# Performance work log

Hardware: AMD Instinct MI355X
Metric: run time of the kernel (lower is better)

Reference implementation:

```python
import jax, jax.numpy as jnp
import numpy as np

LAM = 0.5  # self.lam_
N, T, C, H, W = 8, 8, 128, 64, 64


def setup_inputs() -> dict:
    key = jax.random.key(0)
    k1, k2, k3, k4 = jax.random.split(key, 4)
    x = jax.random.normal(k1, (N, T, C, H, W), dtype=jnp.float32)
    # Conv2d(2,1,k=3,p=1,bias=False) weights: [out=1, in=2, 3, 3]
    w_conv1 = jax.random.normal(k2, (1, 2, 3, 3), dtype=jnp.float32) * 0.1
    w_conv2 = jax.random.normal(k3, (1, 2, 3, 3), dtype=jnp.float32) * 0.1
    # Conv3d(2T, T, k=3, p=1, bias=False): [out=T, in=2T, 3, 3, 3]
    w_conv_last = jax.random.normal(k4, (T, 2 * T, 3, 3, 3), dtype=jnp.float32) * 0.05
    return {"x": x, "w_conv1": w_conv1, "w_conv2": w_conv2, "w_conv_last": w_conv_last}


def _conv2d_same(y, wgt):
    # y: [B, 2, H, W], wgt: [1, 2, 3, 3] -> [B, 1, H, W]
    return jax.lax.conv_general_dilated(
        y, wgt, window_strides=(1, 1), padding=[(1, 1), (1, 1)],
        dimension_numbers=("NCHW", "OIHW", "NCHW"))


def reference(x, w_conv1, w_conv2, w_conv_last):
    n, t, c, h, w = x.shape
    kc = int(c * LAM)
    kt = int(t * LAM)

    # pooled importance map: avg + max over spatial -> [n, t, c]
    M = jnp.mean(x, axis=(3, 4)) + jnp.max(x, axis=(3, 4))

    # --- channel top-k mask ---
    # Faithful to the torch fancy-index scatter loop: important_channels[:, i, topk_[:, i]] = 1
    # broadcasts the write over ALL batch rows, i.e. a per-timestep union over the batch.
    _, topk_c = jax.lax.top_k(M, kc)                                  # [n, t, kc]
    t_ids = jnp.broadcast_to(jnp.arange(t)[None, :, None], topk_c.shape)
    mask_ch = jnp.zeros((t, c), x.dtype).at[t_ids.ravel(), topk_c.ravel()].set(1.0)  # [t, c]

    # --- time top-k mask (on transposed map) ---
    _, topk_t = jax.lax.top_k(jnp.swapaxes(M, 1, 2), kt)              # [n, c, kt]
    c_ids = jnp.broadcast_to(jnp.arange(c)[None, :, None], topk_t.shape)
    mask_tm = jnp.zeros((c, t), x.dtype).at[c_ids.ravel(), topk_t.ravel()].set(1.0).T  # [t, c]

    # important iff (mask_ch + mask_tm)/2 == 0.5  <=> XOR of the two masks
    imp = jnp.where(mask_ch + mask_tm == 1.0, 1.0, 0.0).astype(x.dtype)  # [t, c]
    imp = imp[None, :, :, None, None]                                    # [1, t, c, 1, 1]

    im_feat = imp * x
    sub_feat = x - im_feat  # (1 - imp) * x

    im_avg = jnp.mean(im_feat, axis=2, keepdims=True) / LAM           # [n, t, 1, h, w]
    im_max = jnp.max(im_feat, axis=2, keepdims=True)
    sub_avg = jnp.mean(sub_feat, axis=2, keepdims=True) / (1.0 - LAM)
    sub_max = jnp.max(sub_feat, axis=2, keepdims=True)

    im_x = jnp.concatenate([im_avg, im_max], axis=2)                  # [n, t, 2, h, w]
    sub_x = jnp.concatenate([sub_avg, sub_max], axis=2)

    # SeqToANNContainer flattens (t, n) then conv2d per-sample; flatten order irrelevant.
    im_map = jax.nn.sigmoid(_conv2d_same(im_x.reshape(n * t, 2, h, w), w_conv1)).reshape(n, t, 1, h, w)
    sub_map = jax.nn.sigmoid(_conv2d_same(sub_x.reshape(n * t, 2, h, w), w_conv2)).reshape(n, t, 1, h, w)

    htsa = jnp.concatenate([im_map * im_feat, sub_map * sub_feat], axis=1)  # [n, 2t, c, h, w]

    # Conv3d(2t -> t, k=3, p=1): treats t as channels, c as depth
    out = jax.lax.conv_general_dilated(
        htsa, w_conv_last, window_strides=(1, 1, 1),
        padding=[(1, 1), (1, 1), (1, 1)],
        dimension_numbers=("NCDHW", "OIDHW", "NCDHW"))
    return out  # [n, t, c, h, w]
```

## Files before the change

kernel.cpp:

```cpp
#include <hip/hip_runtime.h>
#include <math.h>

#define NN 8
#define TT 8
#define CC 128
#define HH 64
#define WW 64
#define HW 4096

typedef unsigned int u32;
typedef unsigned short u16;
typedef __attribute__((ext_vector_type(8))) short short8;
typedef __attribute__((ext_vector_type(4))) float floatx4;

__device__ __forceinline__ u16 f2bf(float f){
    u32 u = __float_as_uint(f);
    u32 r = (u + 0x7fffu + ((u >> 16) & 1u)) >> 16;
    return (u16)r;
}
__device__ __forceinline__ float bf2f(u16 h){
    return __uint_as_float(((u32)h) << 16);
}

__global__ __launch_bounds__(256) void k1_M(const float* __restrict__ x, float* __restrict__ M){
    int plane = blockIdx.x * 4 + (threadIdx.x >> 6);
    int lane  = threadIdx.x & 63;
    const float* p = x + (size_t)plane * HW;
    float s = 0.f, mx = -INFINITY;
    #pragma unroll
    for (int it = 0; it < 16; ++it){
        float4 v = *(const float4*)(p + it*256 + lane*4);
        s += v.x + v.y + v.z + v.w;
        mx = fmaxf(mx, fmaxf(fmaxf(v.x, v.y), fmaxf(v.z, v.w)));
    }
    #pragma unroll
    for (int off = 32; off > 0; off >>= 1){
        s += __shfl_xor(s, off, 64);
        mx = fmaxf(mx, __shfl_xor(mx, off, 64));
    }
    if (lane == 0) M[plane] = s * (1.0f/(float)HW) + mx;
}

__global__ __launch_bounds__(128) void k2_imp(const float* __restrict__ M, float* __restrict__ imp){
    int t = blockIdx.x;
    int c = threadIdx.x;
    __shared__ float Ms[NN*CC];
    for (int n = 0; n < NN; ++n)
        Ms[n*CC + c] = M[(n*TT + t)*CC + c];
    __syncthreads();
    bool sel_ch = false;
    for (int n = 0; n < NN; ++n){
        float mv = Ms[n*CC + c];
        int rank = 0;
        for (int c2 = 0; c2 < CC; ++c2){
            float v2 = Ms[n*CC + c2];
            rank += (v2 > mv) || (v2 == mv && c2 < c);
        }
        sel_ch = sel_ch || (rank < 64);
    }
    bool sel_tm = false;
    for (int n = 0; n < NN; ++n){
        float mv = M[(n*TT + t)*CC + c];
        int rank = 0;
        for (int t2 = 0; t2 < TT; ++t2){
            float v2 = M[(n*TT + t2)*CC + c];
            rank += (v2 > mv) || (v2 == mv && t2 < t);
        }
        sel_tm = sel_tm || (rank < 4);
    }
    imp[t*CC + c] = (sel_ch != sel_tm) ? 1.0f : 0.0f;
}

__global__ __launch_bounds__(512) void k3a_stats(const float* __restrict__ x,
        const float* __restrict__ imp, u16* __restrict__ st){
    int nt = blockIdx.x; int t = nt & 7;
    int px = blockIdx.y * 512 + threadIdx.x;
    const float* xp = x + (size_t)nt * CC * HW + px;
    float sa = 0.f, sb = 0.f, ma = -INFINITY, mb = -INFINITY;
    for (int c = 0; c < CC; ++c){
        float ip = imp[t*CC + c];
        float v = xp[c*HW];
        float a = ip*v, b = v - a;
        sa += a; sb += b;
        ma = fmaxf(ma, a); mb = fmaxf(mb, b);
    }
    st[(nt*4+0)*HW + px] = f2bf(sa * (1.f/64.f));
    st[(nt*4+1)*HW + px] = f2bf(ma);
    st[(nt*4+2)*HW + px] = f2bf(sb * (1.f/64.f));
    st[(nt*4+3)*HW + px] = f2bf(mb);
}

__global__ __launch_bounds__(256) void k3b_maps(const u16* __restrict__ st,
        const float* __restrict__ w1, const float* __restrict__ w2,
        float* __restrict__ maps){
    int nt = blockIdx.x;
    int y0 = blockIdx.y * 16;
    __shared__ float S[4*18*66];
    int tid = threadIdx.x;
    for (int idx = tid; idx < 4*18*66; idx += 256){
        int s  = idx / 1188;
        int r  = (idx % 1188) / 66;
        int xx = idx % 66;
        int gy = y0 - 1 + r, gx = xx - 1;
        float v = 0.f;
        if ((u32)gy < HH && (u32)gx < WW)
            v = bf2f(st[(nt*4 + s)*HW + gy*WW + gx]);
        S[idx] = v;
    }
    __syncthreads();
    float wa[18], wb[18];
    #pragma unroll
    for (int i = 0; i < 18; ++i){ wa[i] = w1[i]; wb[i] = w2[i]; }
    for (int k = 0; k < 4; ++k){
        int p = k*256 + tid;
        int y = p >> 6, xx = p & 63;
        float zi = 0.f, zs = 0.f;
        #pragma unroll
        for (int dy = 0; dy < 3; ++dy)
            #pragma unroll
            for (int dx = 0; dx < 3; ++dx){
                int sp = (y+dy)*66 + xx + dx;
                zi += wa[dy*3+dx] * S[sp] + wa[9+dy*3+dx] * S[1188 + sp];
                zs += wb[dy*3+dx] * S[2376 + sp] + wb[9+dy*3+dx] * S[3564 + sp];
            }
        maps[(nt*2+0)*HW + y0*WW + p] = 1.0f / (1.0f + expf(-zi));
        maps[(nt*2+1)*HW + y0*WW + p] = 1.0f / (1.0f + expf(-zs));
    }
}

__global__ __launch_bounds__(256) void k4_xs(const float* __restrict__ x,
        const float* __restrict__ impf, const float* __restrict__ maps,
        u16* __restrict__ xs){
    int c = blockIdx.x;
    int n = blockIdx.y;
    int tid = threadIdx.x;
    const float* mp[TT];
    #pragma unroll
    for (int t = 0; t < TT; ++t){
        float v = impf[t*CC + c];
        mp[t] = maps + ((size_t)((n*TT + t)*2) + (v > 0.f ? 0 : 1)) * HW;
    }
    const float* xb = x + ((size_t)(n*TT)*CC + c) * HW;
    u16* xr = xs + ((size_t)n*CC + c) * HW * 8;
    for (int it = 0; it < 16; ++it){
        int p = it*256 + tid;
        union { u16 h[8]; uint4 v4; } r;
        #pragma unroll
        for (int t = 0; t < TT; ++t){
            float xv = xb[(size_t)t*CC*HW + p];
            r.h[t] = f2bf(xv * mp[t][p]);
        }
        *(uint4*)(xr + (size_t)p*8) = r.v4;
    }
}

__global__ __launch_bounds__(64) void kW_frag(const float* __restrict__ wlast,
        const float* __restrict__ impf, u16* __restrict__ fw){
    int c_out = blockIdx.x;
    int stp   = blockIdx.y;
    int lane  = threadIdx.x;
    int m = lane & 15, q = lane >> 4;
    int tap = 4*stp + q;
    int dc = tap / 9;
    int c_in = c_out - 1 + dc;
    bool valid = (m < 8) && (tap < 27) && ((u32)c_in < CC);
    union { u16 h[8]; uint4 v; } pk;
    #pragma unroll
    for (int j = 0; j < 8; ++j){
        float wv = 0.f;
        if (valid){
            int idx = (impf[j*CC + c_in] > 0.f) ? j : j + 8;
            wv = wlast[(m*16 + idx)*27 + tap];
        }
        pk.h[j] = f2bf(wv);
    }
    *(uint4*)(fw + (((size_t)c_out*7 + stp)*64 + lane)*8) = pk.v;
}

constexpr int offb16(int tap){
    return (((tap/9)*6 + ((tap/3)%3))*66 + (tap%3))*16;
}

__global__ __launch_bounds__(256, 6) void k5_fold(
        const u16* __restrict__ xs, const u16* __restrict__ fw,
        float* __restrict__ out){
    __shared__ __align__(16) u16 ft[1584*8];
    int tid  = threadIdx.x;
    int lane = tid & 63;
    int w    = tid >> 6;
    int c0 = blockIdx.x * 2;
    int y0 = blockIdx.y * 4;
    int n  = blockIdx.z;
    int cl = w & 1;
    int c_out = c0 + cl;

    short8 afr[7];
    const u16* fwb = fw + ((size_t)c_out*7*64 + lane)*8;
    #pragma unroll
    for (int stp = 0; stp < 7; ++stp)
        afr[stp] = *(const short8*)(fwb + stp*512);

    for (int idx = tid; idx < 1584; idx += 256){
        int cc  = idx / 396;
        int rm  = idx % 396;
        int yyl = rm / 66;
        int xx  = rm % 66;
        int gc = c0 - 1 + cc;
        int gy = y0 - 1 + yyl;
        int gx = xx - 1;
        uint4 v = make_uint4(0,0,0,0);
        if ((u32)gc < CC && (u32)gy < HH && (u32)gx < WW)
            v = *(const uint4*)(xs + (((size_t)n*CC + gc)*HW + gy*WW + gx)*8);
        *(uint4*)(ft + idx*8) = v;
    }
    __syncthreads();

    int col = lane & 15;
    int q   = lane >> 4;
    const char* fb = (const char*)ft;
    int offs[7];
    #pragma unroll
    for (int stp = 0; stp < 7; ++stp){
        int tap = 4*stp + q;
        if (tap >= 27) tap = 0;
        offs[stp] = offb16(tap);
    }
    for (int yy = 0; yy < 2; ++yy){
        int yl = (w >> 1)*2 + yy;
        int rowb = ((cl*6 + yl)*66 + col)*16;
        #pragma unroll
        for (int xp = 0; xp < 2; ++xp){
            int b0off = rowb + xp*512;
            int b1off = b0off + 256;
            floatx4 acc0 = {0.f,0.f,0.f,0.f};
            floatx4 acc1 = {0.f,0.f,0.f,0.f};
            #pragma unroll
            for (int stp = 0; stp < 7; ++stp){
                short8 b0 = *(const short8*)(fb + b0off + offs[stp]);
                short8 b1 = *(const short8*)(fb + b1off + offs[stp]);
                acc0 = __builtin_amdgcn_mfma_f32_16x16x32_bf16(afr[stp], b0, acc0, 0, 0, 0);
                acc1 = __builtin_amdgcn_mfma_f32_16x16x32_bf16(afr[stp], b1, acc1, 0, 0, 0);
            }
            if (lane < 32){
                int y = y0 + yl;
                int xa = xp*32 + col;
                #pragma unroll
                for (int rg = 0; rg < 4; ++rg){
                    int o = (lane >> 4)*4 + rg;
                    size_t ob = (((size_t)(n*TT + o))*CC + c_out)*HW + y*WW;
                    out[ob + xa]      = acc0[rg];
                    out[ob + xa + 16] = acc1[rg];
                }
            }
        }
    }
}

template<bool USE_XS>
__global__ __launch_bounds__(256) void k5_conv3d(
        const float* __restrict__ x, const u16* __restrict__ xs,
        const float* __restrict__ impf, const float* __restrict__ wlast,
        const float* __restrict__ maps, float* __restrict__ out){
    __shared__ __align__(16) u16 fim[1584*8];
    __shared__ __align__(16) u16 fsb[1584*8];
    __shared__ u32 maskw[CC*4];
    int tid  = threadIdx.x;
    int lane = tid & 63;
    int w    = tid >> 6;
    int c0 = blockIdx.x * 2;
    int y0 = blockIdx.y * 4;
    int n  = blockIdx.z;

    for (int idx = tid; idx < CC*4; idx += 256){
        int c = idx >> 2, j = idx & 3;
        u32 m = (impf[(2*j)*CC + c]   > 0.f ? 0x0000FFFFu : 0u)
              | (impf[(2*j+1)*CC + c] > 0.f ? 0xFFFF0000u : 0u);
        maskw[idx] = m;
    }

    for (int idx = tid; idx < 896; idx += 256){
        int stp = idx >> 6;
        int l   = idx & 63;
        int m = l & 15, q = l >> 4;
        int i0 = (q & 1) * 8, s = q >> 1;
        int tap = 2*stp + s;
        bool valid = (m < 8) && (tap < 27);
        union { u16 h[8]; uint4 v; } pk;
        #pragma unroll
        for (int j = 0; j < 8; ++j){
            float wv = valid ? wlast[(m*16 + i0 + j)*27 + tap] : 0.f;
            pk.h[j] = f2bf(wv);
        }
        *(uint4*)(fim + idx*8) = pk.v;
    }
    __syncthreads();
    short8 afr[14];
    #pragma unroll
    for (int stp = 0; stp < 14; ++stp)
        afr[stp] = *(const short8*)(fim + (stp*64 + lane)*8);
    __syncthreads();

    for (int idx = tid; idx < 1584; idx += 256){
        int cc  = idx / 396;
        int rm  = idx % 396;
        int yyl = rm / 66;
        int xx  = rm % 66;
        int gc = c0 - 1 + cc;
        int gy = y0 - 1 + yyl;
        int gx = xx - 1;
        uint4 vim = make_uint4(0,0,0,0), vsb = make_uint4(0,0,0,0);
        if ((u32)gc < CC && (u32)gy < HH && (u32)gx < WW){
            int gp = gy*WW + gx;
            u32 al[4];
            if (USE_XS){
                uint4 v = *(const uint4*)(xs + (((size_t)n*CC + gc)*HW + gp)*8);
                al[0] = v.x; al[1] = v.y; al[2] = v.z; al[3] = v.w;
            } else {
                const float* xn  = x    + (((size_t)(n*TT))*CC + gc)*HW + gp;
                const float* mpn = maps + ((size_t)n*TT*2)*HW + gp;
                u16 hv[8];
                #pragma unroll
                for (int t = 0; t < TT; ++t){
                    float ip = impf[t*CC + gc];
                    float xv = xn[(size_t)t*CC*HW];
                    float mv = mpn[((size_t)t*2 + (ip > 0.f ? 0 : 1))*HW];
                    hv[t] = f2bf(xv * mv);
                }
                #pragma unroll
                for (int j = 0; j < 4; ++j)
                    al[j] = (u32)hv[2*j] | ((u32)hv[2*j+1] << 16);
            }
            u32 m0 = maskw[gc*4+0], m1 = maskw[gc*4+1];
            u32 m2 = maskw[gc*4+2], m3 = maskw[gc*4+3];
            vim.x = al[0] & m0; vim.y = al[1] & m1;
            vim.z = al[2] & m2; vim.w = al[3] & m3;
            vsb.x = al[0] ^ vim.x; vsb.y = al[1] ^ vim.y;
            vsb.z = al[2] ^ vim.z; vsb.w = al[3] ^ vim.w;
        }
        *(uint4*)(fim + idx*8) = vim;
        *(uint4*)(fsb + idx*8) = vsb;
    }
    __syncthreads();

    int col = lane & 15;
    int q   = (lane >> 4) & 1;
    int s   = lane >> 5;
    const char* fb = (const char*)(q ? fsb : fim);
    int offs[14];
    #pragma unroll
    for (int stp = 0; stp < 14; ++stp){
        int tap = 2*stp + s;
        if (tap >= 27) tap = 0;
        offs[stp] = offb16(tap);
    }
    int cl = w & 1;
    for (int yy = 0; yy < 2; ++yy){
        int yl = (w >> 1)*2 + yy;
        int rowb = ((cl*6 + yl)*66 + col)*16;
        #pragma unroll
        for (int xp = 0; xp < 2; ++xp){
            int b0off = rowb + xp*512;
            int b1off = b0off + 256;
            floatx4 acc0 = {0.f,0.f,0.f,0.f};
            floatx4 acc1 = {0.f,0.f,0.f,0.f};
            #pragma unroll
            for (int stp = 0; stp < 14; ++stp){
                short8 b0 = *(const short8*)(fb + b0off + offs[stp]);
                short8 b1 = *(const short8*)(fb + b1off + offs[stp]);
                acc0 = __builtin_amdgcn_mfma_f32_16x16x32_bf16(afr[stp], b0, acc0, 0, 0, 0);
                acc1 = __builtin_amdgcn_mfma_f32_16x16x32_bf16(afr[stp], b1, acc1, 0, 0, 0);
            }
            if (lane < 32){
                int c = c0 + cl, y = y0 + yl;
                int xa = xp*32 + col;
                #pragma unroll
                for (int rg = 0; rg < 4; ++rg){
                    int o = (lane >> 4)*4 + rg;
                    size_t ob = (((size_t)(n*TT + o))*CC + c)*HW + y*WW;
                    out[ob + xa]      = acc0[rg];
                    out[ob + xa + 16] = acc1[rg];
                }
            }
        }
    }
}

extern "C" void kernel_launch(void* const* d_in, const int* in_sizes, int n_in,
                              void* d_out, int out_size, void* d_ws, size_t ws_size,
                              hipStream_t stream){
    const float* x     = (const float*)d_in[0];
    const float* w1    = (const float*)d_in[1];
    const float* w2    = (const float*)d_in[2];
    const float* wlast = (const float*)d_in[3];
    float* out = (float*)d_out;

    float* ws   = (float*)d_ws;
    float* M    = ws;
    float* imp  = ws + 8192;
    float* maps = ws + 9216;
    u16*   st   = (u16*)(ws + 9216 + 524288);
    u16*   xs   = (u16*)(ws + 9216 + 524288 + 524288);
    u16*   fw   = st;
    const size_t WS_NEED = (size_t)(9216 + 524288 + 524288) * 4 + (size_t)NN*TT*CC*HW*2;

    k1_M      <<<dim3(NN*TT*CC/4), dim3(256), 0, stream>>>(x, M);
    k2_imp    <<<dim3(TT),         dim3(128), 0, stream>>>(M, imp);
    k3a_stats <<<dim3(NN*TT, 8),   dim3(512), 0, stream>>>(x, imp, st);
    k3b_maps  <<<dim3(NN*TT, 4),   dim3(256), 0, stream>>>(st, w1, w2, maps);
    if (ws_size >= WS_NEED){
        kW_frag <<<dim3(CC, 7), dim3(64),  0, stream>>>(wlast, imp, fw);
        k4_xs   <<<dim3(CC, NN), dim3(256), 0, stream>>>(x, imp, maps, xs);
        k5_fold <<<dim3(CC/2, HH/4, NN), dim3(256), 0, stream>>>(xs, fw, out);
    } else {
        k5_conv3d<false> <<<dim3(CC/2, HH/4, NN), dim3(256), 0, stream>>>(x, xs, imp, wlast, maps, out);
    }
}
```

Measured before the change: 381.3 us.

## Fuse gated bf16 staging into conv3d MFMA kernel and vectorize stats pass

Removes the separate k4_xs pass that wrote a bf16 time-interleaved copy of the gated input to workspace. k5_fuse now reads x and the sigmoid maps directly while filling its shared tile, using per-block precomputed map offsets. The stats kernel also gets float4 loads with four pixels per thread and importance weights cached in shared memory. This saves a full write and re-read of an intermediate tensor. In exchange the conv kernel does strided fp32 gathers across t with halo re-reads, which could make its load phase slower.

```diff
diff --git a/kernel.cpp b/kernel.cpp
--- a/kernel.cpp
+++ b/kernel.cpp
@@ -74,20 +74,38 @@
 __global__ __launch_bounds__(512) void k3a_stats(const float* __restrict__ x,
         const float* __restrict__ imp, u16* __restrict__ st){
     int nt = blockIdx.x; int t = nt & 7;
-    int px = blockIdx.y * 512 + threadIdx.x;
+    int px = (blockIdx.y * 512 + threadIdx.x) * 4;
+    __shared__ float ipr[CC];
+    if (threadIdx.x < CC) ipr[threadIdx.x] = imp[t*CC + threadIdx.x];
+    __syncthreads();
     const float* xp = x + (size_t)nt * CC * HW + px;
-    float sa = 0.f, sb = 0.f, ma = -INFINITY, mb = -INFINITY;
+    float sa[4] = {0,0,0,0}, sb[4] = {0,0,0,0};
+    float ma[4] = {-INFINITY,-INFINITY,-INFINITY,-INFINITY};
+    float mb[4] = {-INFINITY,-INFINITY,-INFINITY,-INFINITY};
     for (int c = 0; c < CC; ++c){
-        float ip = imp[t*CC + c];
-        float v = xp[c*HW];
-        float a = ip*v, b = v - a;
-        sa += a; sb += b;
-        ma = fmaxf(ma, a); mb = fmaxf(mb, b);
-    }
-    st[(nt*4+0)*HW + px] = f2bf(sa * (1.f/64.f));
-    st[(nt*4+1)*HW + px] = f2bf(ma);
-    st[(nt*4+2)*HW + px] = f2bf(sb * (1.f/64.f));
-    st[(nt*4+3)*HW + px] = f2bf(mb);
+        float ip = ipr[c];
+        float4 v = *(const float4*)(xp + (size_t)c*HW);
+        float vv[4] = {v.x, v.y, v.z, v.w};
+        #pragma unroll
+        for (int j = 0; j < 4; ++j){
+            float a = ip*vv[j], b = vv[j] - a;
+            sa[j] += a; sb[j] += b;
+            ma[j] = fmaxf(ma[j], a); mb[j] = fmaxf(mb[j], b);
+        }
+    }
+    union { u16 h[4]; uint2 v2; } o;
+    #pragma unroll
+    for (int j = 0; j < 4; ++j) o.h[j] = f2bf(sa[j] * (1.f/64.f));
+    *(uint2*)(st + (nt*4+0)*HW + px) = o.v2;
+    #pragma unroll
+    for (int j = 0; j < 4; ++j) o.h[j] = f2bf(ma[j]);
+    *(uint2*)(st + (nt*4+1)*HW + px) = o.v2;
+    #pragma unroll
+    for (int j = 0; j < 4; ++j) o.h[j] = f2bf(sb[j] * (1.f/64.f));
+    *(uint2*)(st + (nt*4+2)*HW + px) = o.v2;
+    #pragma unroll
+    for (int j = 0; j < 4; ++j) o.h[j] = f2bf(mb[j]);
+    *(uint2*)(st + (nt*4+3)*HW + px) = o.v2;
 }
 
 __global__ __launch_bounds__(256) void k3b_maps(const u16* __restrict__ st,
@@ -128,32 +146,6 @@
     }
 }
 
-__global__ __launch_bounds__(256) void k4_xs(const float* __restrict__ x,
-        const float* __restrict__ impf, const float* __restrict__ maps,
-        u16* __restrict__ xs){
-    int c = blockIdx.x;
-    int n = blockIdx.y;
-    int tid = threadIdx.x;
-    const float* mp[TT];
-    #pragma unroll
-    for (int t = 0; t < TT; ++t){
-        float v = impf[t*CC + c];
-        mp[t] = maps + ((size_t)((n*TT + t)*2) + (v > 0.f ? 0 : 1)) * HW;
-    }
-    const float* xb = x + ((size_t)(n*TT)*CC + c) * HW;
-    u16* xr = xs + ((size_t)n*CC + c) * HW * 8;
-    for (int it = 0; it < 16; ++it){
-        int p = it*256 + tid;
-        union { u16 h[8]; uint4 v4; } r;
-        #pragma unroll
-        for (int t = 0; t < TT; ++t){
-            float xv = xb[(size_t)t*CC*HW + p];
-            r.h[t] = f2bf(xv * mp[t][p]);
-        }
-        *(uint4*)(xr + (size_t)p*8) = r.v4;
-    }
-}
-
 __global__ __launch_bounds__(64) void kW_frag(const float* __restrict__ wlast,
         const float* __restrict__ impf, u16* __restrict__ fw){
     int c_out = blockIdx.x;
@@ -181,10 +173,12 @@
     return (((tap/9)*6 + ((tap/3)%3))*66 + (tap%3))*16;
 }
 
-__global__ __launch_bounds__(256, 6) void k5_fold(
-        const u16* __restrict__ xs, const u16* __restrict__ fw,
+__global__ __launch_bounds__(256, 6) void k5_fuse(
+        const float* __restrict__ x, const float* __restrict__ impf,
+        const float* __restrict__ maps, const u16* __restrict__ fw,
         float* __restrict__ out){
     __shared__ __align__(16) u16 ft[1584*8];
+    __shared__ u32 mofs[4][8];
     int tid  = threadIdx.x;
     int lane = tid & 63;
     int w    = tid >> 6;
@@ -194,11 +188,19 @@
     int cl = w & 1;
     int c_out = c0 + cl;
 
+    if (tid < 32){
+        int cc = tid >> 3, t = tid & 7;
+        int gc = c0 - 1 + cc;
+        float ip = ((u32)gc < CC) ? impf[t*CC + gc] : 0.f;
+        mofs[cc][t] = (u32)(((n*TT + t)*2 + (ip > 0.f ? 0 : 1)) * HW);
+    }
+
     short8 afr[7];
     const u16* fwb = fw + ((size_t)c_out*7*64 + lane)*8;
     #pragma unroll
     for (int stp = 0; stp < 7; ++stp)
         afr[stp] = *(const short8*)(fwb + stp*512);
+    __syncthreads();
 
     for (int idx = tid; idx < 1584; idx += 256){
         int cc  = idx / 396;
@@ -209,8 +211,22 @@
         int gy = y0 - 1 + yyl;
         int gx = xx - 1;
         uint4 v = make_uint4(0,0,0,0);
-        if ((u32)gc < CC && (u32)gy < HH && (u32)gx < WW)
-            v = *(const uint4*)(xs + (((size_t)n*CC + gc)*HW + gy*WW + gx)*8);
+        if ((u32)gc < CC && (u32)gy < HH && (u32)gx < WW){
+            int gp = gy*WW + gx;
+            const float* xn = x + ((size_t)(n*TT)*CC + gc)*HW + gp;
+            const float* mb = maps + gp;
+            u16 hv[8];
+            #pragma unroll
+            for (int t = 0; t < TT; ++t){
+                float xv = xn[(size_t)t*CC*HW];
+                float mv = mb[mofs[cc][t]];
+                hv[t] = f2bf(xv * mv);
+            }
+            v.x = (u32)hv[0] | ((u32)hv[1] << 16);
+            v.y = (u32)hv[2] | ((u32)hv[3] << 16);
+            v.z = (u32)hv[4] | ((u32)hv[5] << 16);
+            v.w = (u32)hv[6] | ((u32)hv[7] << 16);
+        }
         *(uint4*)(ft + idx*8) = v;
     }
     __syncthreads();
@@ -256,9 +272,8 @@
     }
 }
 
-template<bool USE_XS>
 __global__ __launch_bounds__(256) void k5_conv3d(
-        const float* __restrict__ x, const u16* __restrict__ xs,
+        const float* __restrict__ x,
         const float* __restrict__ impf, const float* __restrict__ wlast,
         const float* __restrict__ maps, float* __restrict__ out){
     __shared__ __align__(16) u16 fim[1584*8];
@@ -312,24 +327,19 @@
         if ((u32)gc < CC && (u32)gy < HH && (u32)gx < WW){
             int gp = gy*WW + gx;
             u32 al[4];
-            if (USE_XS){
-                uint4 v = *(const uint4*)(xs + (((size_t)n*CC + gc)*HW + gp)*8);
-                al[0] = v.x; al[1] = v.y; al[2] = v.z; al[3] = v.w;
-            } else {
-                const float* xn  = x    + (((size_t)(n*TT))*CC + gc)*HW + gp;
-                const float* mpn = maps + ((size_t)n*TT*2)*HW + gp;
-                u16 hv[8];
-                #pragma unroll
-                for (int t = 0; t < TT; ++t){
-                    float ip = impf[t*CC + gc];
-                    float xv = xn[(size_t)t*CC*HW];
-                    float mv = mpn[((size_t)t*2 + (ip > 0.f ? 0 : 1))*HW];
-                    hv[t] = f2bf(xv * mv);
-                }
-                #pragma unroll
-                for (int j = 0; j < 4; ++j)
-                    al[j] = (u32)hv[2*j] | ((u32)hv[2*j+1] << 16);
-            }
+            const float* xn  = x    + ((size_t)(n*TT)*CC + gc)*HW + gp;
+            const float* mpn = maps + ((size_t)n*TT*2)*HW + gp;
+            u16 hv[8];
+            #pragma unroll
+            for (int t = 0; t < TT; ++t){
+                float ip = impf[t*CC + gc];
+                float xv = xn[(size_t)t*CC*HW];
+                float mv = mpn[((size_t)t*2 + (ip > 0.f ? 0 : 1))*HW];
+                hv[t] = f2bf(xv * mv);
+            }
+            #pragma unroll
+            for (int j = 0; j < 4; ++j)
+                al[j] = (u32)hv[2*j] | ((u32)hv[2*j+1] << 16);
             u32 m0 = maskw[gc*4+0], m1 = maskw[gc*4+1];
             u32 m2 = maskw[gc*4+2], m3 = maskw[gc*4+3];
             vim.x = al[0] & m0; vim.y = al[1] & m1;
@@ -399,19 +409,17 @@
     float* imp  = ws + 8192;
     float* maps = ws + 9216;
     u16*   st   = (u16*)(ws + 9216 + 524288);
-    u16*   xs   = (u16*)(ws + 9216 + 524288 + 524288);
     u16*   fw   = st;
-    const size_t WS_NEED = (size_t)(9216 + 524288 + 524288) * 4 + (size_t)NN*TT*CC*HW*2;
+    const size_t WS_MAIN = (size_t)(9216 + 524288 + 524288) * 4;
 
     k1_M      <<<dim3(NN*TT*CC/4), dim3(256), 0, stream>>>(x, M);
     k2_imp    <<<dim3(TT),         dim3(128), 0, stream>>>(M, imp);
-    k3a_stats <<<dim3(NN*TT, 8),   dim3(512), 0, stream>>>(x, imp, st);
+    k3a_stats <<<dim3(NN*TT, 2),   dim3(512), 0, stream>>>(x, imp, st);
     k3b_maps  <<<dim3(NN*TT, 4),   dim3(256), 0, stream>>>(st, w1, w2, maps);
-    if (ws_size >= WS_NEED){
-        kW_frag <<<dim3(CC, 7), dim3(64),  0, stream>>>(wlast, imp, fw);
-        k4_xs   <<<dim3(CC, NN), dim3(256), 0, stream>>>(x, imp, maps, xs);
-        k5_fold <<<dim3(CC/2, HH/4, NN), dim3(256), 0, stream>>>(xs, fw, out);
+    if (ws_size >= WS_MAIN){
+        kW_frag <<<dim3(CC, 7), dim3(64), 0, stream>>>(wlast, imp, fw);
+        k5_fuse <<<dim3(CC/2, HH/4, NN), dim3(256), 0, stream>>>(x, imp, maps, fw, out);
     } else {
-        k5_conv3d<false> <<<dim3(CC/2, HH/4, NN), dim3(256), 0, stream>>>(x, xs, imp, wlast, maps, out);
-    }
-}
+        k5_conv3d <<<dim3(CC/2, HH/4, NN), dim3(256), 0, stream>>>(x, imp, wlast, maps, out);
+    }
+}
```

Result: faster. 349.2 us (-8.4%).
